# Kernel tuning notes

Hardware: AMD Instinct MI355X
Metric: run time of the kernel (lower is better)

The kernel has to match this reference:

```python
import jax, jax.numpy as jnp
import numpy as np

TAU_MIN, TAU_MAX = 1.5, 4.0
NUM_EXPERTS, TOP_K = 8, 2
V_TH = 1.0
BN_EPS = 1e-5
SG_ALPHA = 4.0  # spikingjelly Sigmoid surrogate default

@jax.custom_vjp
def spike(v):
    # Heaviside spike with sigmoid surrogate gradient
    return (v >= 0.0).astype(v.dtype)

def _spike_fwd(v):
    return spike(v), v

def _spike_bwd(v, g):
    s = jax.nn.sigmoid(SG_ALPHA * v)
    return (g * SG_ALPHA * s * (1.0 - s),)

spike.defvjp(_spike_fwd, _spike_bwd)

def lif(x, tau):
    # MultiStepLIFNode, v_reset=0 (hard reset), detach_reset=True. x: (T, ...)
    def step(v, xt):
        v = v + (xt - v) / tau          # charge
        s = spike(v - V_TH)             # fire
        v = v * (1.0 - jax.lax.stop_gradient(s))  # detached hard reset
        return v, s
    return jax.lax.scan(step, jnp.zeros_like(x[0]), x)[1]

def conv1x1(x, W, b):
    # x: (T,B,Cin,H,W), W: (Cout,Cin) -> (T,B,Cout,H,W)
    return jnp.einsum('tbchw,oc->tbohw', x, W) + b[None, None, :, None, None]

def bn_eval(x, scale, bias):
    # eval-mode BatchNorm2d with running_mean=0, running_var=1
    inv = scale / jnp.sqrt(1.0 + BN_EPS)
    return x * inv[None, None, :, None, None] + bias[None, None, :, None, None]

def expert_fwd(x, tau, W1, b1, s1, bb1, W2, b2, s2, bb2):
    # MS_MLP_Expert: LIF -> conv1x1 -> BN -> (+res) -> LIF -> conv1x1 -> BN -> (+res)
    identity = x
    h = lif(x, tau)
    h = bn_eval(conv1x1(h, W1, b1), s1, bb1)
    h = identity + h            # res: in_features == hidden_features
    identity = h
    o = lif(h, tau)
    o = bn_eval(conv1x1(o, W2, b2), s2, bb2)
    return o + identity

def moe_forward(x, router_W, router_b, router_bn_scale, router_bn_bias,
                W1, b1, bn1_scale, bn1_bias, W2, b2, bn2_scale, bn2_bias):
    T, B, C, H, W = x.shape
    taus = jnp.linspace(TAU_MIN, TAU_MAX, NUM_EXPERTS).astype(x.dtype)
    # --- SpikeRouter ---
    r = lif(x, 2.0)
    r = bn_eval(conv1x1(r, router_W, router_b), router_bn_scale, router_bn_bias)  # (T,B,E,H,W)
    logits_tb = r.mean(axis=(-2, -1))          # (T,B,E)
    # batch-level temporal routing: aggregate logits over T
    logits = logits_tb.mean(axis=0)            # (B,E)
    probs = jax.nn.softmax(logits, axis=-1)
    topw, topi = jax.lax.top_k(probs, TOP_K)   # (B,k)
    topw = topw / topw.sum(axis=-1, keepdims=True)
    dense_w = jnp.zeros((B, NUM_EXPERTS), dtype=x.dtype).at[
        jnp.arange(B)[:, None], topi].set(topw)  # (B,E)
    # --- experts: each processes the full temporal sequence ---
    ys = jax.vmap(expert_fwd, in_axes=(None, 0, 0, 0, 0, 0, 0, 0, 0, 0))(
        x, taus, W1, b1, bn1_scale, bn1_bias, W2, b2, bn2_scale, bn2_bias)  # (E,T,B,C,H,W)
    out = jnp.einsum('etbchw,be->tbchw', ys, dense_w)
    return out

def setup_inputs() -> dict:
    key = jax.random.key(0)
    ks = jax.random.split(key, 6)
    T, B, C, H, Wd = 4, 16, 384, 16, 16
    E = NUM_EXPERTS
    wscale = 1.0 / np.sqrt(C)
    return {
        'x': jax.random.normal(ks[0], (T, B, C, H, Wd), jnp.float32),
        'router_W': jax.random.normal(ks[1], (E, C), jnp.float32) * wscale,
        'router_b': jnp.zeros((E,), jnp.float32),
        'router_bn_scale': jnp.ones((E,), jnp.float32),
        'router_bn_bias': jnp.zeros((E,), jnp.float32),
        'W1': jax.random.normal(ks[2], (E, C, C), jnp.float32) * wscale,
        'b1': jnp.zeros((E, C), jnp.float32),
        'bn1_scale': jnp.ones((E, C), jnp.float32),
        'bn1_bias': jnp.zeros((E, C), jnp.float32),
        'W2': jax.random.normal(ks[3], (E, C, C), jnp.float32) * wscale,
        'b2': jnp.zeros((E, C), jnp.float32),
        'bn2_scale': jnp.ones((E, C), jnp.float32),
        'bn2_bias': jnp.zeros((E, C), jnp.float32),
    }

def reference(x, router_W, router_b, router_bn_scale, router_bn_bias,
              W1, b1, bn1_scale, bn1_bias, W2, b2, bn2_scale, bn2_bias):
    return moe_forward(x, router_W, router_b, router_bn_scale, router_bn_bias,
                       W1, b1, bn1_scale, bn1_bias, W2, b2, bn2_scale, bn2_bias)
```

## Files before the change

kernel.cpp:

```cpp
#include <hip/hip_runtime.h>
#include <math.h>

#define T_  4
#define B_  16
#define C_  384
#define HW_ 256
#define E_  8

typedef __attribute__((ext_vector_type(8))) __bf16 bf16x8;
typedef __attribute__((ext_vector_type(4))) float f32x4;

union FragU { uint4 u; bf16x8 v; };

__device__ __forceinline__ float tau_of(int e) {
    if (e == 7) return 4.0f;
    const float delta = 2.5f / 7.0f;
    return __fadd_rn(1.5f, __fmul_rn((float)e, delta));
}

__device__ __forceinline__ FragU expand_mask(unsigned m) {
    FragU f;
    f.u.x = ((m & 1u)   ? 0x3F80u : 0u) | ((m & 2u)   ? 0x3F800000u : 0u);
    f.u.y = ((m & 4u)   ? 0x3F80u : 0u) | ((m & 8u)   ? 0x3F800000u : 0u);
    f.u.z = ((m & 16u)  ? 0x3F80u : 0u) | ((m & 32u)  ? 0x3F800000u : 0u);
    f.u.w = ((m & 64u)  ? 0x3F80u : 0u) | ((m & 128u) ? 0x3F800000u : 0u);
    return f;
}

__global__ __launch_bounds__(256) void k_prep(const float* __restrict__ x,
        const float* __restrict__ W1, const float* __restrict__ W2,
        unsigned short* __restrict__ Whif, unsigned short* __restrict__ Wlof,
        float* __restrict__ m) {
    if (blockIdx.x < 1152) {
        int tid = blockIdx.x * 256 + threadIdx.x;
        int l = tid & 63;
        int f = tid >> 6;
        int osub = f % 24;
        int ksub = (f / 24) % 12;
        int cv = (f / 288) & 1;
        int e = f / 576;
        const float* Wsrc = (cv == 0 ? W1 : W2) + (size_t)e * C_ * C_;
        int o = osub * 16 + (l & 15);
        int c0 = ksub * 32 + (l >> 4) * 8;
        const float* src = Wsrc + (size_t)o * C_ + c0;
        unsigned hw[8], lw[8];
#pragma unroll
        for (int j = 0; j < 8; ++j) {
            float w = src[j];
            unsigned u = __float_as_uint(w);
            unsigned hi = (u + 0x7FFFu + ((u >> 16) & 1u)) >> 16;
            float hf = __uint_as_float(hi << 16);
            float res = __fsub_rn(w, hf);
            unsigned ru = __float_as_uint(res);
            unsigned lo = (ru + 0x7FFFu + ((ru >> 16) & 1u)) >> 16;
            hw[j] = hi & 0xFFFFu;
            lw[j] = lo & 0xFFFFu;
        }
        size_t dst = (size_t)f * 512 + (size_t)l * 8;
        uint4 hv = make_uint4(hw[0] | (hw[1] << 16), hw[2] | (hw[3] << 16),
                              hw[4] | (hw[5] << 16), hw[6] | (hw[7] << 16));
        uint4 lv = make_uint4(lw[0] | (lw[1] << 16), lw[2] | (lw[3] << 16),
                              lw[4] | (lw[5] << 16), lw[6] | (lw[7] << 16));
        *reinterpret_cast<uint4*>(Whif + dst) = hv;
        *reinterpret_cast<uint4*>(Wlof + dst) = lv;
    } else {
        int bc = blockIdx.x - 1152;
        int b = bc / C_, c = bc % C_;
        int p = threadIdx.x;
        int wv = threadIdx.x >> 6;
        __shared__ int cnt[T_][4];
        float v = 0.0f;
#pragma unroll
        for (int t = 0; t < T_; ++t) {
            float xv = x[((t * B_ + b) * C_ + c) * HW_ + p];
            v = __fadd_rn(v, __fdiv_rn(__fsub_rn(xv, v), 2.0f));
            bool s = (__fsub_rn(v, 1.0f) >= 0.0f);
            if (s) v = 0.0f;
            unsigned long long mask = __ballot(s);
            if ((threadIdx.x & 63) == 0) cnt[t][wv] = (int)__popcll(mask);
        }
        __syncthreads();
        if (threadIdx.x < T_) {
            int t = threadIdx.x;
            int tot = cnt[t][0] + cnt[t][1] + cnt[t][2] + cnt[t][3];
            m[(t * B_ + b) * C_ + c] = (float)tot * 0.00390625f;
        }
    }
}

__device__ __forceinline__ void conv_mfma(const unsigned short* __restrict__ Whif,
                                          const unsigned short* __restrict__ Wlof,
                                          unsigned base,
                                          const unsigned char* __restrict__ sm,
                                          f32x4 (&acc)[3][4],
                                          int tw, int lane, int q, int pl) {
    const unsigned lane8 = (unsigned)lane * 8u;
    const unsigned wbase = base + (unsigned)(tw * 3) * 512u + lane8;
    FragU c0f, c1f, c2f, n0f, n1f, n2f;
    c0f.u = *reinterpret_cast<const uint4*>(Wlof + wbase);
    c1f.u = *reinterpret_cast<const uint4*>(Wlof + wbase + 512u);
    c2f.u = *reinterpret_cast<const uint4*>(Wlof + wbase + 1024u);
#pragma unroll 1
    for (int ksub = 0; ksub < 12; ++ksub) {
        unsigned fo = wbase + (unsigned)ksub * 24u * 512u;
        FragU bf[T_];
#pragma unroll
        for (int t = 0; t < T_; ++t) {
            unsigned mbyte = sm[(t * 16 + pl) * 48 + ksub * 4 + q];
            bf[t] = expand_mask(mbyte);
        }
        n0f.u = *reinterpret_cast<const uint4*>(Whif + fo);
        n1f.u = *reinterpret_cast<const uint4*>(Whif + fo + 512u);
        n2f.u = *reinterpret_cast<const uint4*>(Whif + fo + 1024u);
#pragma unroll
        for (int t = 0; t < T_; ++t) {
            acc[0][t] = __builtin_amdgcn_mfma_f32_16x16x32_bf16(c0f.v, bf[t].v, acc[0][t], 0, 0, 0);
            acc[1][t] = __builtin_amdgcn_mfma_f32_16x16x32_bf16(c1f.v, bf[t].v, acc[1][t], 0, 0, 0);
            acc[2][t] = __builtin_amdgcn_mfma_f32_16x16x32_bf16(c2f.v, bf[t].v, acc[2][t], 0, 0, 0);
        }
        if (ksub < 11) {
            unsigned fn = fo + 24u * 512u;
            c0f.u = *reinterpret_cast<const uint4*>(Wlof + fn);
            c1f.u = *reinterpret_cast<const uint4*>(Wlof + fn + 512u);
            c2f.u = *reinterpret_cast<const uint4*>(Wlof + fn + 1024u);
        }
#pragma unroll
        for (int t = 0; t < T_; ++t) {
            acc[0][t] = __builtin_amdgcn_mfma_f32_16x16x32_bf16(n0f.v, bf[t].v, acc[0][t], 0, 0, 0);
            acc[1][t] = __builtin_amdgcn_mfma_f32_16x16x32_bf16(n1f.v, bf[t].v, acc[1][t], 0, 0, 0);
            acc[2][t] = __builtin_amdgcn_mfma_f32_16x16x32_bf16(n2f.v, bf[t].v, acc[2][t], 0, 0, 0);
        }
    }
}

__global__ __launch_bounds__(1024, 4) void k_expert(
        const float* __restrict__ x, const float* __restrict__ m,
        const float* __restrict__ rW, const float* __restrict__ rb,
        const float* __restrict__ rbs, const float* __restrict__ rbb,
        const unsigned short* __restrict__ Whif, const unsigned short* __restrict__ Wlof,
        const float* __restrict__ b1, const float* __restrict__ s1sc, const float* __restrict__ s1bi,
        const float* __restrict__ b2, const float* __restrict__ s2sc, const float* __restrict__ s2bi,
        float* __restrict__ out) {
    int blk = blockIdx.x;
    int b = (blk & 7) | (((blk >> 3) & 1) << 3);
    int ptile = blk >> 4;

    __shared__ unsigned char s1m[2][T_ * 16 * 48];
    __shared__ unsigned char s2m[2][T_ * 16 * 48];
    __shared__ float bns[2 * 6 * C_];
    __shared__ float lds_part[512 * 49];
    __shared__ float lg[E_];
    __shared__ float wsl[2];
    __shared__ int esl[2];

    int tid = threadIdx.x;
    int team = tid >> 9;
    int tid2 = tid & 511;
    int tw = tid2 >> 6;
    int lane = tid & 63;
    int q = lane >> 4;
    int pl = lane & 15;
    int p = ptile * 16 + pl;
    float denom = sqrtf(__fadd_rn(1.0f, 1e-5f));

    if (tid < 64) {
        int combo = tid & 31, half = tid >> 5;
        int e = combo >> 2, t = combo & 3;
        float dot = 0.0f;
        int c0 = half * 192;
        for (int c = 0; c < 192; ++c)
            dot = fmaf(rW[e * C_ + c0 + c], m[(t * B_ + b) * C_ + c0 + c], dot);
        dot += __shfl_down(dot, 32);
        float Ar = __fdiv_rn(rbs[e], denom);
        float lt = __fadd_rn(__fmul_rn(__fadd_rn(dot, rb[e]), Ar), rbb[e]);
        lt = __fadd_rn(lt, __shfl_xor(lt, 1));
        lt = __fadd_rn(lt, __shfl_xor(lt, 2));
        if (half == 0 && t == 0) lg[e] = __fmul_rn(lt, 0.25f);
    }
    __syncthreads();
    if (tid == 0) {
        float pr[E_];
        float mx = lg[0];
        for (int i = 1; i < E_; ++i) mx = fmaxf(mx, lg[i]);
        float s = 0.0f;
        for (int i = 0; i < E_; ++i) { pr[i] = expf(__fsub_rn(lg[i], mx)); s = __fadd_rn(s, pr[i]); }
        for (int i = 0; i < E_; ++i) pr[i] = __fdiv_rn(pr[i], s);
        int i0 = 0;
        for (int i = 1; i < E_; ++i) if (pr[i] > pr[i0]) i0 = i;
        int i1 = (i0 == 0) ? 1 : 0;
        for (int i = 0; i < E_; ++i) if (i != i0 && pr[i] > pr[i1]) i1 = i;
        float s2 = __fadd_rn(pr[i0], pr[i1]);
        wsl[0] = __fdiv_rn(pr[i0], s2);
        wsl[1] = __fdiv_rn(pr[i1], s2);
        esl[0] = i0;
        esl[1] = i1;
    }
    __syncthreads();

    int er = esl[team];
    float wgt = wsl[team];
    float tau = tau_of(er);

    if (tid < 2 * C_) {
        int r_ = tid / C_;
        int o = tid % C_;
        int eo = esl[r_] * C_ + o;
        bns[(r_ * 6 + 0) * C_ + o] = __fdiv_rn(s1sc[eo], denom);
        bns[(r_ * 6 + 1) * C_ + o] = b1[eo];
        bns[(r_ * 6 + 2) * C_ + o] = s1bi[eo];
        bns[(r_ * 6 + 3) * C_ + o] = __fdiv_rn(s2sc[eo], denom);
        bns[(r_ * 6 + 4) * C_ + o] = b2[eo];
        bns[(r_ * 6 + 5) * C_ + o] = s2bi[eo];
    }

#pragma unroll 1
    for (int task = tid2; task < 48 * 16; task += 512) {
        int cb = task >> 4;
        int tpl = task & 15;
        int tp = ptile * 16 + tpl;
        float v[8];
#pragma unroll
        for (int j = 0; j < 8; ++j) v[j] = 0.0f;
#pragma unroll
        for (int t = 0; t < T_; ++t) {
            int gbase = ((t * B_ + b) * C_ + cb * 8) * HW_ + tp;
            unsigned mb = 0;
#pragma unroll
            for (int j = 0; j < 8; ++j) {
                float xv = x[gbase + j * HW_];
                v[j] = __fadd_rn(v[j], __fdiv_rn(__fsub_rn(xv, v[j]), tau));
                if (__fsub_rn(v[j], 1.0f) >= 0.0f) { mb |= (1u << j); v[j] = 0.0f; }
            }
            s1m[team][(t * 16 + tpl) * 48 + cb] = (unsigned char)mb;
        }
    }
    __syncthreads();

    const unsigned base1 = (unsigned)(er * 2) * 12u * 24u * 512u;
    const unsigned base2 = (unsigned)(er * 2 + 1) * 12u * 24u * 512u;

    {
        f32x4 acc[3][4];
#pragma unroll
        for (int os = 0; os < 3; ++os)
#pragma unroll
            for (int t = 0; t < T_; ++t) acc[os][t] = (f32x4)0.0f;

        conv_mfma(Whif, Wlof, base1, &s1m[team][0], acc, tw, lane, q, pl);

#pragma unroll
        for (int os = 0; os < 3; ++os) {
            float v2s[4] = {0.f, 0.f, 0.f, 0.f};
#pragma unroll
            for (int t = 0; t < T_; ++t) {
                unsigned nb = 0;
#pragma unroll
                for (int r = 0; r < 4; ++r) {
                    int o = tw * 48 + os * 16 + q * 4 + r;
                    int gi = ((t * B_ + b) * C_ + o) * HW_ + p;
                    float y = acc[os][t][r];
                    float h = __fadd_rn(x[gi],
                        __fadd_rn(__fmul_rn(__fadd_rn(y, bns[(team * 6 + 1) * C_ + o]),
                                            bns[(team * 6 + 0) * C_ + o]),
                                  bns[(team * 6 + 2) * C_ + o]));
                    float contrib = __fmul_rn(wgt, h);
                    if (team == 0) out[gi] = contrib;
                    else lds_part[tid2 * 49 + os * 16 + t * 4 + r] = contrib;
                    v2s[r] = __fadd_rn(v2s[r], __fdiv_rn(__fsub_rn(h, v2s[r]), tau));
                    if (__fsub_rn(v2s[r], 1.0f) >= 0.0f) { nb |= (1u << r); v2s[r] = 0.f; }
                }
                unsigned nb_hi = (unsigned)__shfl_down((int)nb, 16);
                if ((q & 1) == 0) {
                    int cbyte = tw * 6 + os * 2 + (q >> 1);
                    s2m[team][(t * 16 + pl) * 48 + cbyte] = (unsigned char)(nb | (nb_hi << 4));
                }
            }
        }
    }
    __syncthreads();

    {
        f32x4 acc[3][4];
#pragma unroll
        for (int os = 0; os < 3; ++os)
#pragma unroll
            for (int t = 0; t < T_; ++t) acc[os][t] = (f32x4)0.0f;

        conv_mfma(Whif, Wlof, base2, &s2m[team][0], acc, tw, lane, q, pl);

#pragma unroll
        for (int os = 0; os < 3; ++os)
#pragma unroll
            for (int t = 0; t < T_; ++t)
#pragma unroll
                for (int r = 0; r < 4; ++r) {
                    int o = tw * 48 + os * 16 + q * 4 + r;
                    float y = acc[os][t][r];
                    float val = __fmul_rn(wgt,
                        __fadd_rn(__fmul_rn(__fadd_rn(y, bns[(team * 6 + 4) * C_ + o]),
                                            bns[(team * 6 + 3) * C_ + o]),
                                  bns[(team * 6 + 5) * C_ + o]));
                    if (team == 1) {
                        int li = tid2 * 49 + os * 16 + t * 4 + r;
                        lds_part[li] = __fadd_rn(lds_part[li], val);
                    } else {
                        acc[os][t][r] = val;
                    }
                }
        __syncthreads();

        if (team == 0) {
#pragma unroll
            for (int os = 0; os < 3; ++os)
#pragma unroll
                for (int t = 0; t < T_; ++t)
#pragma unroll
                    for (int r = 0; r < 4; ++r) {
                        int o = tw * 48 + os * 16 + q * 4 + r;
                        int gi = ((t * B_ + b) * C_ + o) * HW_ + p;
                        float pp = lds_part[tid2 * 49 + os * 16 + t * 4 + r];
                        out[gi] = __fadd_rn(__fadd_rn(out[gi], acc[os][t][r]), pp);
                    }
        }
    }
}

extern "C" void kernel_launch(void* const* d_in, const int* in_sizes, int n_in,
                              void* d_out, int out_size, void* d_ws, size_t ws_size,
                              hipStream_t stream) {
    const float* x    = (const float*)d_in[0];
    const float* rW   = (const float*)d_in[1];
    const float* rb   = (const float*)d_in[2];
    const float* rbs  = (const float*)d_in[3];
    const float* rbb  = (const float*)d_in[4];
    const float* W1   = (const float*)d_in[5];
    const float* b1   = (const float*)d_in[6];
    const float* s1sc = (const float*)d_in[7];
    const float* s1bi = (const float*)d_in[8];
    const float* W2   = (const float*)d_in[9];
    const float* b2   = (const float*)d_in[10];
    const float* s2sc = (const float*)d_in[11];
    const float* s2bi = (const float*)d_in[12];
    float* out = (float*)d_out;

    unsigned short* Whif = (unsigned short*)d_ws;
    unsigned short* Wlof = Whif + 2359296;
    float* m = (float*)((char*)d_ws + 9437184);

    hipLaunchKernelGGL(k_prep, dim3(1152 + B_ * C_), dim3(256), 0, stream,
                       x, W1, W2, Whif, Wlof, m);
    hipLaunchKernelGGL(k_expert, dim3(256), dim3(1024), 0, stream,
                       x, m, rW, rb, rbs, rbb, Whif, Wlof,
                       b1, s1sc, s1bi, b2, s2sc, s2bi, out);
}
```

Before: 182.0 us.

## Merge prep work into fewer larger blocks and keep expert partials in LDS

The prep kernel becomes 256 blocks of 1024 threads. Each block grid-strides over the weight hi/lo split and computes router spike counts for 24 (b,c) pairs, with six loads in flight per thread and LDS atomics for the counts. The expert kernel no longer writes the first-stage contribution to global memory and reads it back. Team 0 now adds it into an LDS sum buffer, and the final output is written once. This removes a global read-modify-write and a large launch, at the cost of an extra barrier and LDS accumulation passes.

Measured after the change: 173.3 us. 4.8% less time.

```diff
diff --git a/kernel.cpp b/kernel.cpp
--- a/kernel.cpp
+++ b/kernel.cpp
@@ -27,14 +27,15 @@
     return f;
 }
 
-__global__ __launch_bounds__(256) void k_prep(const float* __restrict__ x,
+__global__ __launch_bounds__(1024) void k_prep(const float* __restrict__ x,
         const float* __restrict__ W1, const float* __restrict__ W2,
         unsigned short* __restrict__ Whif, unsigned short* __restrict__ Wlof,
         float* __restrict__ m) {
-    if (blockIdx.x < 1152) {
-        int tid = blockIdx.x * 256 + threadIdx.x;
-        int l = tid & 63;
-        int f = tid >> 6;
+    int tid = threadIdx.x;
+    int gt = blockIdx.x * 1024 + tid;
+    for (int task = gt; task < 294912; task += 262144) {
+        int l = task & 63;
+        int f = task >> 6;
         int osub = f % 24;
         int ksub = (f / 24) % 12;
         int cv = (f / 288) & 1;
@@ -63,28 +64,45 @@
                               lw[4] | (lw[5] << 16), lw[6] | (lw[7] << 16));
         *reinterpret_cast<uint4*>(Whif + dst) = hv;
         *reinterpret_cast<uint4*>(Wlof + dst) = lv;
-    } else {
-        int bc = blockIdx.x - 1152;
+    }
+    int p = tid & 255;
+    int slot = tid >> 8;
+    int lane = tid & 63;
+    __shared__ int cnt[4][6][T_];
+    if (tid < 96) (&cnt[0][0][0])[tid] = 0;
+    __syncthreads();
+    float v[6];
+    int bs[6], cs[6];
+#pragma unroll
+    for (int it = 0; it < 6; ++it) {
+        v[it] = 0.0f;
+        int bc = blockIdx.x * 4 + slot + it * 1024;
+        bs[it] = bc / C_;
+        cs[it] = bc % C_;
+    }
+#pragma unroll
+    for (int t = 0; t < T_; ++t) {
+        float xv[6];
+#pragma unroll
+        for (int it = 0; it < 6; ++it)
+            xv[it] = x[((t * B_ + bs[it]) * C_ + cs[it]) * HW_ + p];
+#pragma unroll
+        for (int it = 0; it < 6; ++it) {
+            v[it] = __fadd_rn(v[it], __fdiv_rn(__fsub_rn(xv[it], v[it]), 2.0f));
+            bool s = (__fsub_rn(v[it], 1.0f) >= 0.0f);
+            if (s) v[it] = 0.0f;
+            unsigned long long mask = __ballot(s);
+            if (lane == 0) atomicAdd(&cnt[slot][it][t], (int)__popcll(mask));
+        }
+    }
+    __syncthreads();
+    if (tid < 96) {
+        int slot2 = tid / 24;
+        int rem = tid % 24;
+        int it = rem >> 2, t = rem & 3;
+        int bc = blockIdx.x * 4 + slot2 + it * 1024;
         int b = bc / C_, c = bc % C_;
-        int p = threadIdx.x;
-        int wv = threadIdx.x >> 6;
-        __shared__ int cnt[T_][4];
-        float v = 0.0f;
-#pragma unroll
-        for (int t = 0; t < T_; ++t) {
-            float xv = x[((t * B_ + b) * C_ + c) * HW_ + p];
-            v = __fadd_rn(v, __fdiv_rn(__fsub_rn(xv, v), 2.0f));
-            bool s = (__fsub_rn(v, 1.0f) >= 0.0f);
-            if (s) v = 0.0f;
-            unsigned long long mask = __ballot(s);
-            if ((threadIdx.x & 63) == 0) cnt[t][wv] = (int)__popcll(mask);
-        }
-        __syncthreads();
-        if (threadIdx.x < T_) {
-            int t = threadIdx.x;
-            int tot = cnt[t][0] + cnt[t][1] + cnt[t][2] + cnt[t][3];
-            m[(t * B_ + b) * C_ + c] = (float)tot * 0.00390625f;
-        }
+        m[(t * B_ + b) * C_ + c] = (float)cnt[slot2][it][t] * 0.00390625f;
     }
 }
 
@@ -148,7 +166,7 @@
     __shared__ unsigned char s1m[2][T_ * 16 * 48];
     __shared__ unsigned char s2m[2][T_ * 16 * 48];
     __shared__ float bns[2 * 6 * C_];
-    __shared__ float lds_part[512 * 49];
+    __shared__ float lds_sum[512 * 49];
     __shared__ float lg[E_];
     __shared__ float wsl[2];
     __shared__ int esl[2];
@@ -239,89 +257,98 @@
     const unsigned base1 = (unsigned)(er * 2) * 12u * 24u * 512u;
     const unsigned base2 = (unsigned)(er * 2 + 1) * 12u * 24u * 512u;
 
-    {
-        f32x4 acc[3][4];
+    f32x4 acc[3][4];
+
+#pragma unroll
+    for (int os = 0; os < 3; ++os)
+#pragma unroll
+        for (int t = 0; t < T_; ++t) acc[os][t] = (f32x4)0.0f;
+
+    conv_mfma(Whif, Wlof, base1, &s1m[team][0], acc, tw, lane, q, pl);
+
+#pragma unroll
+    for (int os = 0; os < 3; ++os) {
+        float v2s[4] = {0.f, 0.f, 0.f, 0.f};
+#pragma unroll
+        for (int t = 0; t < T_; ++t) {
+            unsigned nb = 0;
+#pragma unroll
+            for (int r = 0; r < 4; ++r) {
+                int o = tw * 48 + os * 16 + q * 4 + r;
+                int gi = ((t * B_ + b) * C_ + o) * HW_ + p;
+                float y = acc[os][t][r];
+                float h = __fadd_rn(x[gi],
+                    __fadd_rn(__fmul_rn(__fadd_rn(y, bns[(team * 6 + 1) * C_ + o]),
+                                        bns[(team * 6 + 0) * C_ + o]),
+                              bns[(team * 6 + 2) * C_ + o]));
+                float contrib = __fmul_rn(wgt, h);
+                acc[os][t][r] = contrib;
+                if (team == 1) lds_sum[tid2 * 49 + os * 16 + t * 4 + r] = contrib;
+                v2s[r] = __fadd_rn(v2s[r], __fdiv_rn(__fsub_rn(h, v2s[r]), tau));
+                if (__fsub_rn(v2s[r], 1.0f) >= 0.0f) { nb |= (1u << r); v2s[r] = 0.f; }
+            }
+            unsigned nb_hi = (unsigned)__shfl_down((int)nb, 16);
+            if ((q & 1) == 0) {
+                int cbyte = tw * 6 + os * 2 + (q >> 1);
+                s2m[team][(t * 16 + pl) * 48 + cbyte] = (unsigned char)(nb | (nb_hi << 4));
+            }
+        }
+    }
+    __syncthreads();
+
+    if (team == 0) {
 #pragma unroll
         for (int os = 0; os < 3; ++os)
 #pragma unroll
-            for (int t = 0; t < T_; ++t) acc[os][t] = (f32x4)0.0f;
-
-        conv_mfma(Whif, Wlof, base1, &s1m[team][0], acc, tw, lane, q, pl);
-
-#pragma unroll
-        for (int os = 0; os < 3; ++os) {
-            float v2s[4] = {0.f, 0.f, 0.f, 0.f};
-#pragma unroll
-            for (int t = 0; t < T_; ++t) {
-                unsigned nb = 0;
+            for (int t = 0; t < T_; ++t)
+#pragma unroll
+                for (int r = 0; r < 4; ++r) {
+                    int li = tid2 * 49 + os * 16 + t * 4 + r;
+                    lds_sum[li] = __fadd_rn(lds_sum[li], acc[os][t][r]);
+                }
+    }
+    __syncthreads();
+
+#pragma unroll
+    for (int os = 0; os < 3; ++os)
+#pragma unroll
+        for (int t = 0; t < T_; ++t) acc[os][t] = (f32x4)0.0f;
+
+    conv_mfma(Whif, Wlof, base2, &s2m[team][0], acc, tw, lane, q, pl);
+
+#pragma unroll
+    for (int os = 0; os < 3; ++os)
+#pragma unroll
+        for (int t = 0; t < T_; ++t)
+#pragma unroll
+            for (int r = 0; r < 4; ++r) {
+                int o = tw * 48 + os * 16 + q * 4 + r;
+                float y = acc[os][t][r];
+                float val = __fmul_rn(wgt,
+                    __fadd_rn(__fmul_rn(__fadd_rn(y, bns[(team * 6 + 4) * C_ + o]),
+                                        bns[(team * 6 + 3) * C_ + o]),
+                              bns[(team * 6 + 5) * C_ + o]));
+                if (team == 1) {
+                    int li = tid2 * 49 + os * 16 + t * 4 + r;
+                    lds_sum[li] = __fadd_rn(lds_sum[li], val);
+                } else {
+                    acc[os][t][r] = val;
+                }
+            }
+    __syncthreads();
+
+    if (team == 0) {
+#pragma unroll
+        for (int os = 0; os < 3; ++os)
+#pragma unroll
+            for (int t = 0; t < T_; ++t)
 #pragma unroll
                 for (int r = 0; r < 4; ++r) {
                     int o = tw * 48 + os * 16 + q * 4 + r;
                     int gi = ((t * B_ + b) * C_ + o) * HW_ + p;
-                    float y = acc[os][t][r];
-                    float h = __fadd_rn(x[gi],
-                        __fadd_rn(__fmul_rn(__fadd_rn(y, bns[(team * 6 + 1) * C_ + o]),
-                                            bns[(team * 6 + 0) * C_ + o]),
-                                  bns[(team * 6 + 2) * C_ + o]));
-                    float contrib = __fmul_rn(wgt, h);
-                    if (team == 0) out[gi] = contrib;
-                    else lds_part[tid2 * 49 + os * 16 + t * 4 + r] = contrib;
-                    v2s[r] = __fadd_rn(v2s[r], __fdiv_rn(__fsub_rn(h, v2s[r]), tau));
-                    if (__fsub_rn(v2s[r], 1.0f) >= 0.0f) { nb |= (1u << r); v2s[r] = 0.f; }
+                    float pp = lds_sum[tid2 * 49 + os * 16 + t * 4 + r];
+                    out[gi] = __fadd_rn(pp, acc[os][t][r]);
                 }
-                unsigned nb_hi = (unsigned)__shfl_down((int)nb, 16);
-                if ((q & 1) == 0) {
-                    int cbyte = tw * 6 + os * 2 + (q >> 1);
-                    s2m[team][(t * 16 + pl) * 48 + cbyte] = (unsigned char)(nb | (nb_hi << 4));
-                }
-            }
-        }
-    }
-    __syncthreads();
-
-    {
-        f32x4 acc[3][4];
-#pragma unroll
-        for (int os = 0; os < 3; ++os)
-#pragma unroll
-            for (int t = 0; t < T_; ++t) acc[os][t] = (f32x4)0.0f;
-
-        conv_mfma(Whif, Wlof, base2, &s2m[team][0], acc, tw, lane, q, pl);
-
-#pragma unroll
-        for (int os = 0; os < 3; ++os)
-#pragma unroll
-            for (int t = 0; t < T_; ++t)
-#pragma unroll
-                for (int r = 0; r < 4; ++r) {
-                    int o = tw * 48 + os * 16 + q * 4 + r;
-                    float y = acc[os][t][r];
-                    float val = __fmul_rn(wgt,
-                        __fadd_rn(__fmul_rn(__fadd_rn(y, bns[(team * 6 + 4) * C_ + o]),
-                                            bns[(team * 6 + 3) * C_ + o]),
-                                  bns[(team * 6 + 5) * C_ + o]));
-                    if (team == 1) {
-                        int li = tid2 * 49 + os * 16 + t * 4 + r;
-                        lds_part[li] = __fadd_rn(lds_part[li], val);
-                    } else {
-                        acc[os][t][r] = val;
-                    }
-                }
-        __syncthreads();
-
-        if (team == 0) {
-#pragma unroll
-            for (int os = 0; os < 3; ++os)
-#pragma unroll
-                for (int t = 0; t < T_; ++t)
-#pragma unroll
-                    for (int r = 0; r < 4; ++r) {
-                        int o = tw * 48 + os * 16 + q * 4 + r;
-                        int gi = ((t * B_ + b) * C_ + o) * HW_ + p;
-                        float pp = lds_part[tid2 * 49 + os * 16 + t * 4 + r];
-                        out[gi] = __fadd_rn(__fadd_rn(out[gi], acc[os][t][r]), pp);
-                    }
-        }
     }
 }
 
@@ -347,7 +374,7 @@
     unsigned short* Wlof = Whif + 2359296;
     float* m = (float*)((char*)d_ws + 9437184);
 
-    hipLaunchKernelGGL(k_prep, dim3(1152 + B_ * C_), dim3(256), 0, stream,
+    hipLaunchKernelGGL(k_prep, dim3(256), dim3(1024), 0, stream,
                        x, W1, W2, Whif, Wlof, m);
     hipLaunchKernelGGL(k_expert, dim3(256), dim3(1024), 0, stream,
                        x, m, rW, rb, rbs, rbb, Whif, Wlof,
```
